# Optimization experiments

Measured on AMD Instinct MI355X. Metric: run time of the kernel, lower is better.

Reference implementation:

```python
import jax, jax.numpy as jnp
import numpy as np

S = 4  # upsample scale


def setup_inputs() -> dict:
    key = jax.random.key(0)
    ks = jax.random.split(key, 8)
    B, C, H, W = 4, 128, 64, 64
    feat_lr = jax.random.normal(ks[0], (B, C, H, W), dtype=jnp.float32)
    # gate: Conv2d(C, C//4, 1, bias=False) -> LeakyReLU(0.2) -> Conv2d(C//4, 1, 1, bias=True) -> Sigmoid
    gate_w1 = jax.random.normal(ks[1], (C, C // 4), dtype=jnp.float32) * 0.05
    gate_w2 = jax.random.normal(ks[2], (C // 4, 1), dtype=jnp.float32) * 0.1
    gate_b2 = jnp.full((1,), -3.0, dtype=jnp.float32)  # init bias per module
    # mlp: Conv2d(C+2, C, 1) -> ReLU -> Conv2d(C, C, 1)
    mlp_w1 = jax.random.normal(ks[3], (C + 2, C), dtype=jnp.float32) * 0.05
    mlp_b1 = jax.random.normal(ks[4], (C,), dtype=jnp.float32) * 0.01
    mlp_w2 = jax.random.normal(ks[5], (C, C), dtype=jnp.float32) * 0.05
    mlp_b2 = jax.random.normal(ks[6], (C,), dtype=jnp.float32) * 0.01
    return {"feat_lr": feat_lr, "gate_w1": gate_w1, "gate_w2": gate_w2,
            "gate_b2": gate_b2, "mlp_w1": mlp_w1, "mlp_b1": mlp_b1,
            "mlp_w2": mlp_w2, "mlp_b2": mlp_b2}


def reference(feat_lr, gate_w1, gate_w2, gate_b2, mlp_w1, mlp_b1, mlp_w2, mlp_b2):
    B, C, H, W = feat_lr.shape
    f = jnp.transpose(feat_lr, (0, 2, 3, 1))  # (B,H,W,C)

    # ---- gate on LR grid (1x1 convs == per-pixel matmuls) ----
    g = f @ gate_w1                              # (B,H,W,C//4)
    g = jnp.where(g >= 0, g, 0.2 * g)            # LeakyReLU(0.2)
    gate = jax.nn.sigmoid(g @ gate_w2 + gate_b2) # (B,H,W,1)

    # ---- subpixel grid: channels [x, y], values in (-1,1) ----
    coords = jnp.linspace(-1.0 + 1.0 / S, 1.0 - 1.0 / S, S, dtype=feat_lr.dtype)
    yy, xx = jnp.meshgrid(coords, coords, indexing="ij")
    grid = jnp.stack([xx, yy], axis=-1)          # (S,S,2)

    # ---- mlp: split first conv weight into feat part and grid part.
    # Since convs are 1x1 and feat_hr is nearest-upsampled (constant over each
    # SxS block) while grid tiles per block, hidden = relu(f@W1f + grid@W1g + b1)
    # broadcast over (block, subpixel) — avoids materializing concat/HR inputs.
    w1_f, w1_g = mlp_w1[:C], mlp_w1[C:]          # (C,C), (2,C)
    h_f = f @ w1_f                               # (B,H,W,C)
    h_g = grid @ w1_g                            # (S,S,C)
    hidden = jax.nn.relu(h_f[:, :, None, :, None, :]
                         + h_g[None, None, :, None, :, :]
                         + mlp_b1)               # (B,H,S,W,S,C)
    res = hidden @ mlp_w2 + mlp_b2               # (B,H,S,W,S,C)

    out = res * gate[:, :, None, :, None, :]     # broadcast gate over block
    out = out.reshape(B, H * S, W * S, C)
    return jnp.transpose(out, (0, 3, 1, 2))      # (B,C,H*S,W*S)
```

## Files before the change

kernel.cpp:

```cpp
#include <hip/hip_runtime.h>
#include <hip/hip_bf16.h>
#include <math.h>


typedef __attribute__((ext_vector_type(8))) short bf16x8;
typedef __attribute__((ext_vector_type(4))) float f32x4;

__device__ inline short f2bf(float v) {
    __hip_bfloat16 b = __float2bfloat16(v);
    return *reinterpret_cast<short*>(&b);
}

__global__ __launch_bounds__(256) void w2t_kernel(const float* __restrict__ w2,
                                                  __hip_bfloat16* __restrict__ w2t) {
    __shared__ float tile[16][17];
    const int kt = (blockIdx.x & 7) * 16, jt = (blockIdx.x >> 3) * 16;
    const int tx = threadIdx.x & 15, ty = threadIdx.x >> 4;
    tile[ty][tx] = w2[(kt + ty) * 128 + jt + tx];
    __syncthreads();
    w2t[(jt + ty) * 128 + kt + tx] = __float2bfloat16(tile[tx][ty]);
}

__global__ __launch_bounds__(256, 3) void ipi_kernel(
    const float* __restrict__ feat,
    const float* __restrict__ gate_w1,
    const float* __restrict__ gate_w2,
    const float* __restrict__ gate_b2,
    const float* __restrict__ mlp_w1,
    const float* __restrict__ mlp_b1,
    const float* __restrict__ mlp_b2,
    const __hip_bfloat16* __restrict__ w2t,
    float* __restrict__ out)
{
    __shared__ float hf[16 * 132];
    __shared__ float hgb[16 * 132];
    __shared__ float gate_s[16];
    __shared__ char  hid[32768];
    float* f_tile = (float*)hid;
    float* glds   = (float*)(hid + 8192);

    const int t    = threadIdx.x;
    const int lane = t & 63;
    const int wv   = t >> 6;
    const int bx   = blockIdx.x;
    const int w0   = (bx & 3) * 16;
    const int h    = (bx >> 2) & 63;
    const int b    = bx >> 8;

    bf16x8 afrag[2][4];
    f32x4  b2v[2];
    {
        const __hip_bfloat16* base = w2t + (wv * 32 + (lane & 15)) * 128 + (lane >> 4) * 8;
        #pragma unroll
        for (int jt = 0; jt < 2; ++jt) {
            #pragma unroll
            for (int ks = 0; ks < 4; ++ks)
                afrag[jt][ks] = *(const bf16x8*)(base + jt * 16 * 128 + ks * 32);
            b2v[jt] = *(const f32x4*)&mlp_b2[wv * 32 + jt * 16 + (lane >> 4) * 4];
        }
    }

    {
        const float* fbase = feat + ((size_t)(b * 128) * 64 + h) * 64 + w0;
        #pragma unroll
        for (int i = 0; i < 8; ++i) {
            int idx = t + i * 256;
            int c = idx >> 4, w = idx & 15;
            f_tile[c * 16 + w] = fbase[(size_t)c * 4096 + w];
        }
        #pragma unroll
        for (int i = 0; i < 8; ++i) {
            int idx = t + i * 256;
            int s = idx >> 7, k = idx & 127;
            float cx = -0.75f + 0.5f * (float)(s & 3);
            float cy = -0.75f + 0.5f * (float)(s >> 2);
            hgb[s * 132 + k] = cx * mlp_w1[128 * 128 + k]
                             + cy * mlp_w1[129 * 128 + k]
                             + mlp_b1[k];
        }
    }
    __syncthreads();

    {
        int jg = t & 31, wq = t >> 5;
        float a0 = 0.f, a1 = 0.f;
        for (int c = 0; c < 128; ++c) {
            float gw = gate_w1[c * 32 + jg];
            a0 = fmaf(f_tile[c * 16 + wq], gw, a0);
            a1 = fmaf(f_tile[c * 16 + wq + 8], gw, a1);
        }
        glds[wq * 32 + jg]       = (a0 >= 0.f) ? a0 : 0.2f * a0;
        glds[(wq + 8) * 32 + jg] = (a1 >= 0.f) ? a1 : 0.2f * a1;
    }

    {
        int j = t & 127, wb = t >> 7;
        float acc[8];
        #pragma unroll
        for (int i = 0; i < 8; ++i) acc[i] = 0.f;
        for (int c = 0; c < 128; ++c) {
            float wvv = mlp_w1[c * 128 + j];
            const float4* fp = (const float4*)&f_tile[c * 16 + wb * 8];
            float4 fa = fp[0], fb = fp[1];
            acc[0] = fmaf(fa.x, wvv, acc[0]);
            acc[1] = fmaf(fa.y, wvv, acc[1]);
            acc[2] = fmaf(fa.z, wvv, acc[2]);
            acc[3] = fmaf(fa.w, wvv, acc[3]);
            acc[4] = fmaf(fb.x, wvv, acc[4]);
            acc[5] = fmaf(fb.y, wvv, acc[5]);
            acc[6] = fmaf(fb.z, wvv, acc[6]);
            acc[7] = fmaf(fb.w, wvv, acc[7]);
        }
        #pragma unroll
        for (int i = 0; i < 8; ++i) hf[(wb * 8 + i) * 132 + j] = acc[i];
    }
    __syncthreads();

    if (t < 16) {
        float s = gate_b2[0];
        for (int jg = 0; jg < 32; ++jg) s += glds[t * 32 + jg] * gate_w2[jg];
        gate_s[t] = 1.f / (1.f + expf(-s));
    }

    for (int half = 0; half < 2; ++half) {
        __syncthreads();

        {
            const int mh = t >> 1;
            const int w  = (mh >> 2) & 15;
            const int s  = ((((half << 7) + mh) >> 6) << 2) | (mh & 3);
            const float* hfr = hf  + w * 132 + (t & 1) * 64;
            const float* hgr = hgb + s * 132 + (t & 1) * 64;
            char* rowp = hid + mh * 256;
            const int kb0 = (t & 1) * 128;
            const int sw  = (mh & 7) << 4;
            #pragma unroll
            for (int kc = 0; kc < 8; ++kc) {
                float4 a0 = *(const float4*)(hfr + kc * 8);
                float4 a1 = *(const float4*)(hfr + kc * 8 + 4);
                float4 g0 = *(const float4*)(hgr + kc * 8);
                float4 g1 = *(const float4*)(hgr + kc * 8 + 4);
                bf16x8 hv;
                hv[0] = f2bf(fmaxf(a0.x + g0.x, 0.f));
                hv[1] = f2bf(fmaxf(a0.y + g0.y, 0.f));
                hv[2] = f2bf(fmaxf(a0.z + g0.z, 0.f));
                hv[3] = f2bf(fmaxf(a0.w + g0.w, 0.f));
                hv[4] = f2bf(fmaxf(a1.x + g1.x, 0.f));
                hv[5] = f2bf(fmaxf(a1.y + g1.y, 0.f));
                hv[6] = f2bf(fmaxf(a1.z + g1.z, 0.f));
                hv[7] = f2bf(fmaxf(a1.w + g1.w, 0.f));
                *(bf16x8*)(rowp + ((kb0 + kc * 16) ^ sw)) = hv;
            }
        }
        __syncthreads();

        for (int mt = 0; mt < 8; ++mt) {
            const int mrow = mt * 16 + (lane & 15);
            const int swb  = (mrow & 7) << 4;
            const char* rowp = hid + mrow * 256;
            bf16x8 bfrag[4];
            #pragma unroll
            for (int ks = 0; ks < 4; ++ks)
                bfrag[ks] = *(const bf16x8*)(rowp + ((ks * 64 + (lane >> 4) * 16) ^ swb));

            f32x4 acc0 = {0.f, 0.f, 0.f, 0.f};
            f32x4 acc1 = {0.f, 0.f, 0.f, 0.f};
            #pragma unroll
            for (int ks = 0; ks < 4; ++ks) {
                acc0 = __builtin_amdgcn_mfma_f32_16x16x32_bf16(afrag[0][ks], bfrag[ks], acc0, 0, 0, 0);
                acc1 = __builtin_amdgcn_mfma_f32_16x16x32_bf16(afrag[1][ks], bfrag[ks], acc1, 0, 0, 0);
            }

            const int m  = (half << 7) + mrow;
            const int sy = m >> 6;
            const float g = gate_s[(m >> 2) & 15];
            float* outp = out + ((size_t)(b * 128 + wv * 32 + (lane >> 4) * 4) << 16)
                              + (size_t)(h * 4 + sy) * 256 + w0 * 4 + (m & 63);
            #pragma unroll
            for (int r = 0; r < 4; ++r) {
                outp[(size_t)r << 16]        = (acc0[r] + b2v[0][r]) * g;
                outp[(size_t)(r + 16) << 16] = (acc1[r] + b2v[1][r]) * g;
            }
        }
    }
}

extern "C" void kernel_launch(void* const* d_in, const int* in_sizes, int n_in,
                              void* d_out, int out_size, void* d_ws, size_t ws_size,
                              hipStream_t stream) {
    const float* feat = (const float*)d_in[0];
    const float* gw1  = (const float*)d_in[1];
    const float* gw2  = (const float*)d_in[2];
    const float* gb2  = (const float*)d_in[3];
    const float* w1   = (const float*)d_in[4];
    const float* b1   = (const float*)d_in[5];
    const float* w2   = (const float*)d_in[6];
    const float* b2   = (const float*)d_in[7];
    float* o = (float*)d_out;
    __hip_bfloat16* w2t = (__hip_bfloat16*)d_ws;

    w2t_kernel<<<dim3(64), dim3(256), 0, stream>>>(w2, w2t);
    ipi_kernel<<<dim3(1024), dim3(256), 0, stream>>>(feat, gw1, gw2, gb2, w1, b1, b2, w2t, o);
}
```

Baseline: 55.35 us.

## Split fused kernel into staging and MFMA main kernels via workspace

Splits the fused kernel into two launches. A stage kernel computes the per-pixel first-layer MLP output, the gate, the grid bias term and the transposed bf16 W2, and writes them to workspace. A main kernel reads those values from global memory, builds the hidden tile in LDS and runs the MFMA GEMM. The aim is lower LDS and register use per kernel so occupancy can rise to 4 blocks per CU, and fewer launches by folding the W2 transpose into the stage kernel. The cost is an extra round trip of roughly 8 MB through global memory for hf, and it falls back to the old monolithic path if the workspace is too small.

```diff
diff --git a/kernel.cpp b/kernel.cpp
--- a/kernel.cpp
+++ b/kernel.cpp
@@ -11,72 +11,58 @@
     return *reinterpret_cast<short*>(&b);
 }
 
-__global__ __launch_bounds__(256) void w2t_kernel(const float* __restrict__ w2,
-                                                  __hip_bfloat16* __restrict__ w2t) {
-    __shared__ float tile[16][17];
-    const int kt = (blockIdx.x & 7) * 16, jt = (blockIdx.x >> 3) * 16;
-    const int tx = threadIdx.x & 15, ty = threadIdx.x >> 4;
-    tile[ty][tx] = w2[(kt + ty) * 128 + jt + tx];
-    __syncthreads();
-    w2t[(jt + ty) * 128 + kt + tx] = __float2bfloat16(tile[tx][ty]);
-}
-
-__global__ __launch_bounds__(256, 3) void ipi_kernel(
+__device__ inline void barrier_lgkm() {
+    asm volatile("s_waitcnt lgkmcnt(0)" ::: "memory");
+    __builtin_amdgcn_s_barrier();
+    asm volatile("" ::: "memory");
+}
+
+__global__ __launch_bounds__(256, 4) void ipi_stage_kernel(
     const float* __restrict__ feat,
     const float* __restrict__ gate_w1,
     const float* __restrict__ gate_w2,
     const float* __restrict__ gate_b2,
     const float* __restrict__ mlp_w1,
     const float* __restrict__ mlp_b1,
-    const float* __restrict__ mlp_b2,
-    const __hip_bfloat16* __restrict__ w2t,
-    float* __restrict__ out)
+    const float* __restrict__ w2,
+    float* __restrict__ hf_ws,
+    float* __restrict__ gate_ws,
+    float* __restrict__ hgb_ws,
+    __hip_bfloat16* __restrict__ w2t)
 {
-    __shared__ float hf[16 * 132];
-    __shared__ float hgb[16 * 132];
-    __shared__ float gate_s[16];
-    __shared__ char  hid[32768];
-    float* f_tile = (float*)hid;
-    float* glds   = (float*)(hid + 8192);
-
-    const int t    = threadIdx.x;
-    const int lane = t & 63;
-    const int wv   = t >> 6;
-    const int bx   = blockIdx.x;
-    const int w0   = (bx & 3) * 16;
-    const int h    = (bx >> 2) & 63;
-    const int b    = bx >> 8;
-
-    bf16x8 afrag[2][4];
-    f32x4  b2v[2];
-    {
-        const __hip_bfloat16* base = w2t + (wv * 32 + (lane & 15)) * 128 + (lane >> 4) * 8;
-        #pragma unroll
-        for (int jt = 0; jt < 2; ++jt) {
-            #pragma unroll
-            for (int ks = 0; ks < 4; ++ks)
-                afrag[jt][ks] = *(const bf16x8*)(base + jt * 16 * 128 + ks * 32);
-            b2v[jt] = *(const f32x4*)&mlp_b2[wv * 32 + jt * 16 + (lane >> 4) * 4];
-        }
-    }
-
-    {
-        const float* fbase = feat + ((size_t)(b * 128) * 64 + h) * 64 + w0;
-        #pragma unroll
-        for (int i = 0; i < 8; ++i) {
-            int idx = t + i * 256;
-            int c = idx >> 4, w = idx & 15;
-            f_tile[c * 16 + w] = fbase[(size_t)c * 4096 + w];
-        }
+    __shared__ float f_tile[128 * 16];
+    __shared__ float glds[16 * 32];
+
+    const int t  = threadIdx.x;
+    const int bx = blockIdx.x;
+    const int w0 = (bx & 3) * 16;
+    const int h  = (bx >> 2) & 63;
+    const int b  = bx >> 8;
+
+    if (bx == 0) {
         #pragma unroll
         for (int i = 0; i < 8; ++i) {
             int idx = t + i * 256;
             int s = idx >> 7, k = idx & 127;
             float cx = -0.75f + 0.5f * (float)(s & 3);
             float cy = -0.75f + 0.5f * (float)(s >> 2);
-            hgb[s * 132 + k] = cx * mlp_w1[128 * 128 + k]
-                             + cy * mlp_w1[129 * 128 + k]
-                             + mlp_b1[k];
+            hgb_ws[idx] = cx * mlp_w1[128 * 128 + k]
+                        + cy * mlp_w1[129 * 128 + k]
+                        + mlp_b1[k];
+        }
+    } else if (bx <= 64) {
+        int gid = (bx - 1) * 256 + t;
+        int j = gid >> 7, k = gid & 127;
+        w2t[gid] = __float2bfloat16(w2[k * 128 + j]);
+    }
+
+    {
+        const float* fbase = feat + ((size_t)(b * 128) * 64 + h) * 64 + w0;
+        #pragma unroll
+        for (int i = 0; i < 8; ++i) {
+            int idx = t + i * 256;
+            int c = idx >> 4, w = idx & 15;
+            f_tile[c * 16 + w] = fbase[(size_t)c * 4096 + w];
         }
     }
     __syncthreads();
@@ -111,26 +97,62 @@
             acc[6] = fmaf(fb.z, wvv, acc[6]);
             acc[7] = fmaf(fb.w, wvv, acc[7]);
         }
-        #pragma unroll
-        for (int i = 0; i < 8; ++i) hf[(wb * 8 + i) * 132 + j] = acc[i];
+        float* hfb = hf_ws + ((size_t)((b * 64 + h) * 64) + w0 + wb * 8) * 128 + j;
+        #pragma unroll
+        for (int i = 0; i < 8; ++i) hfb[i * 128] = acc[i];
     }
     __syncthreads();
 
     if (t < 16) {
         float s = gate_b2[0];
         for (int jg = 0; jg < 32; ++jg) s += glds[t * 32 + jg] * gate_w2[jg];
-        gate_s[t] = 1.f / (1.f + expf(-s));
-    }
+        gate_ws[(b * 64 + h) * 64 + w0 + t] = 1.f / (1.f + expf(-s));
+    }
+}
+
+__global__ __launch_bounds__(256, 4) void ipi_main_kernel(
+    const __hip_bfloat16* __restrict__ w2t,
+    const float* __restrict__ mlp_b2,
+    const float* __restrict__ hf_ws,
+    const float* __restrict__ gate_ws,
+    const float* __restrict__ hgb_ws,
+    float* __restrict__ out)
+{
+    __shared__ char hid[32768];
+
+    const int t    = threadIdx.x;
+    const int lane = t & 63;
+    const int wv   = t >> 6;
+    const int bx   = blockIdx.x;
+    const int w0   = (bx & 3) * 16;
+    const int h    = (bx >> 2) & 63;
+    const int b    = bx >> 8;
+
+    bf16x8 afrag[2][4];
+    f32x4  b2v[2];
+    {
+        const __hip_bfloat16* base = w2t + (wv * 32 + (lane & 15)) * 128 + (lane >> 4) * 8;
+        #pragma unroll
+        for (int jt = 0; jt < 2; ++jt) {
+            #pragma unroll
+            for (int ks = 0; ks < 4; ++ks)
+                afrag[jt][ks] = *(const bf16x8*)(base + jt * 16 * 128 + ks * 32);
+            b2v[jt] = *(const f32x4*)&mlp_b2[wv * 32 + jt * 16 + (lane >> 4) * 4];
+        }
+    }
+
+    const float* hfbase = hf_ws + ((size_t)((b * 64 + h) * 64) + w0) * 128;
+    const float* gbase  = gate_ws + (b * 64 + h) * 64 + w0;
 
     for (int half = 0; half < 2; ++half) {
-        __syncthreads();
+        barrier_lgkm();
 
         {
             const int mh = t >> 1;
             const int w  = (mh >> 2) & 15;
-            const int s  = ((((half << 7) + mh) >> 6) << 2) | (mh & 3);
-            const float* hfr = hf  + w * 132 + (t & 1) * 64;
-            const float* hgr = hgb + s * 132 + (t & 1) * 64;
+            const int s  = (((half << 1) + (mh >> 6)) << 2) | (mh & 3);
+            const float* hfr = hfbase + w * 128 + (t & 1) * 64;
+            const float* hgr = hgb_ws + s * 128 + (t & 1) * 64;
             char* rowp = hid + mh * 256;
             const int kb0 = (t & 1) * 128;
             const int sw  = (mh & 7) << 4;
@@ -152,7 +174,7 @@
                 *(bf16x8*)(rowp + ((kb0 + kc * 16) ^ sw)) = hv;
             }
         }
-        __syncthreads();
+        barrier_lgkm();
 
         for (int mt = 0; mt < 8; ++mt) {
             const int mrow = mt * 16 + (lane & 15);
@@ -171,6 +193,166 @@
                 acc1 = __builtin_amdgcn_mfma_f32_16x16x32_bf16(afrag[1][ks], bfrag[ks], acc1, 0, 0, 0);
             }
 
+            const int m  = (half << 7) + mrow;
+            const int sy = m >> 6;
+            const float g = gbase[(m >> 2) & 15];
+            float* outp = out + ((size_t)(b * 128 + wv * 32 + (lane >> 4) * 4) << 16)
+                              + (size_t)(h * 4 + sy) * 256 + w0 * 4 + (m & 63);
+            #pragma unroll
+            for (int r = 0; r < 4; ++r) {
+                outp[(size_t)r << 16]        = (acc0[r] + b2v[0][r]) * g;
+                outp[(size_t)(r + 16) << 16] = (acc1[r] + b2v[1][r]) * g;
+            }
+        }
+    }
+}
+
+__global__ __launch_bounds__(256) void w2t_kernel(const float* __restrict__ w2,
+                                                  __hip_bfloat16* __restrict__ w2t) {
+    __shared__ float tile[16][17];
+    const int kt = (blockIdx.x & 7) * 16, jt = (blockIdx.x >> 3) * 16;
+    const int tx = threadIdx.x & 15, ty = threadIdx.x >> 4;
+    tile[ty][tx] = w2[(kt + ty) * 128 + jt + tx];
+    __syncthreads();
+    w2t[(jt + ty) * 128 + kt + tx] = __float2bfloat16(tile[tx][ty]);
+}
+
+__global__ __launch_bounds__(256, 3) void ipi_mono_kernel(
+    const float* __restrict__ feat, const float* __restrict__ gate_w1,
+    const float* __restrict__ gate_w2, const float* __restrict__ gate_b2,
+    const float* __restrict__ mlp_w1, const float* __restrict__ mlp_b1,
+    const float* __restrict__ mlp_b2, const __hip_bfloat16* __restrict__ w2t,
+    float* __restrict__ out)
+{
+    __shared__ float hf[16 * 132];
+    __shared__ float hgb[16 * 132];
+    __shared__ float gate_s[16];
+    __shared__ char  hid[32768];
+    float* f_tile = (float*)hid;
+    float* glds   = (float*)(hid + 8192);
+
+    const int t    = threadIdx.x;
+    const int lane = t & 63;
+    const int wv   = t >> 6;
+    const int bx   = blockIdx.x;
+    const int w0   = (bx & 3) * 16;
+    const int h    = (bx >> 2) & 63;
+    const int b    = bx >> 8;
+
+    bf16x8 afrag[2][4];
+    f32x4  b2v[2];
+    {
+        const __hip_bfloat16* base = w2t + (wv * 32 + (lane & 15)) * 128 + (lane >> 4) * 8;
+        #pragma unroll
+        for (int jt = 0; jt < 2; ++jt) {
+            #pragma unroll
+            for (int ks = 0; ks < 4; ++ks)
+                afrag[jt][ks] = *(const bf16x8*)(base + jt * 16 * 128 + ks * 32);
+            b2v[jt] = *(const f32x4*)&mlp_b2[wv * 32 + jt * 16 + (lane >> 4) * 4];
+        }
+    }
+    {
+        const float* fbase = feat + ((size_t)(b * 128) * 64 + h) * 64 + w0;
+        #pragma unroll
+        for (int i = 0; i < 8; ++i) {
+            int idx = t + i * 256;
+            int c = idx >> 4, w = idx & 15;
+            f_tile[c * 16 + w] = fbase[(size_t)c * 4096 + w];
+        }
+        #pragma unroll
+        for (int i = 0; i < 8; ++i) {
+            int idx = t + i * 256;
+            int s = idx >> 7, k = idx & 127;
+            float cx = -0.75f + 0.5f * (float)(s & 3);
+            float cy = -0.75f + 0.5f * (float)(s >> 2);
+            hgb[s * 132 + k] = cx * mlp_w1[128 * 128 + k]
+                             + cy * mlp_w1[129 * 128 + k] + mlp_b1[k];
+        }
+    }
+    __syncthreads();
+    {
+        int jg = t & 31, wq = t >> 5;
+        float a0 = 0.f, a1 = 0.f;
+        for (int c = 0; c < 128; ++c) {
+            float gw = gate_w1[c * 32 + jg];
+            a0 = fmaf(f_tile[c * 16 + wq], gw, a0);
+            a1 = fmaf(f_tile[c * 16 + wq + 8], gw, a1);
+        }
+        glds[wq * 32 + jg]       = (a0 >= 0.f) ? a0 : 0.2f * a0;
+        glds[(wq + 8) * 32 + jg] = (a1 >= 0.f) ? a1 : 0.2f * a1;
+    }
+    {
+        int j = t & 127, wb = t >> 7;
+        float acc[8];
+        #pragma unroll
+        for (int i = 0; i < 8; ++i) acc[i] = 0.f;
+        for (int c = 0; c < 128; ++c) {
+            float wvv = mlp_w1[c * 128 + j];
+            const float4* fp = (const float4*)&f_tile[c * 16 + wb * 8];
+            float4 fa = fp[0], fb = fp[1];
+            acc[0] = fmaf(fa.x, wvv, acc[0]);
+            acc[1] = fmaf(fa.y, wvv, acc[1]);
+            acc[2] = fmaf(fa.z, wvv, acc[2]);
+            acc[3] = fmaf(fa.w, wvv, acc[3]);
+            acc[4] = fmaf(fb.x, wvv, acc[4]);
+            acc[5] = fmaf(fb.y, wvv, acc[5]);
+            acc[6] = fmaf(fb.z, wvv, acc[6]);
+            acc[7] = fmaf(fb.w, wvv, acc[7]);
+        }
+        #pragma unroll
+        for (int i = 0; i < 8; ++i) hf[(wb * 8 + i) * 132 + j] = acc[i];
+    }
+    __syncthreads();
+    if (t < 16) {
+        float s = gate_b2[0];
+        for (int jg = 0; jg < 32; ++jg) s += glds[t * 32 + jg] * gate_w2[jg];
+        gate_s[t] = 1.f / (1.f + expf(-s));
+    }
+    for (int half = 0; half < 2; ++half) {
+        __syncthreads();
+        {
+            const int mh = t >> 1;
+            const int w  = (mh >> 2) & 15;
+            const int s  = ((((half << 7) + mh) >> 6) << 2) | (mh & 3);
+            const float* hfr = hf  + w * 132 + (t & 1) * 64;
+            const float* hgr = hgb + s * 132 + (t & 1) * 64;
+            char* rowp = hid + mh * 256;
+            const int kb0 = (t & 1) * 128;
+            const int sw  = (mh & 7) << 4;
+            #pragma unroll
+            for (int kc = 0; kc < 8; ++kc) {
+                float4 a0 = *(const float4*)(hfr + kc * 8);
+                float4 a1 = *(const float4*)(hfr + kc * 8 + 4);
+                float4 g0 = *(const float4*)(hgr + kc * 8);
+                float4 g1 = *(const float4*)(hgr + kc * 8 + 4);
+                bf16x8 hv;
+                hv[0] = f2bf(fmaxf(a0.x + g0.x, 0.f));
+                hv[1] = f2bf(fmaxf(a0.y + g0.y, 0.f));
+                hv[2] = f2bf(fmaxf(a0.z + g0.z, 0.f));
+                hv[3] = f2bf(fmaxf(a0.w + g0.w, 0.f));
+                hv[4] = f2bf(fmaxf(a1.x + g1.x, 0.f));
+                hv[5] = f2bf(fmaxf(a1.y + g1.y, 0.f));
+                hv[6] = f2bf(fmaxf(a1.z + g1.z, 0.f));
+                hv[7] = f2bf(fmaxf(a1.w + g1.w, 0.f));
+                *(bf16x8*)(rowp + ((kb0 + kc * 16) ^ sw)) = hv;
+            }
+        }
+        __syncthreads();
+        for (int mt = 0; mt < 8; ++mt) {
+            const int mrow = mt * 16 + (lane & 15);
+            const int swb  = (mrow & 7) << 4;
+            const char* rowp = hid + mrow * 256;
+            bf16x8 bfrag[4];
+            #pragma unroll
+            for (int ks = 0; ks < 4; ++ks)
+                bfrag[ks] = *(const bf16x8*)(rowp + ((ks * 64 + (lane >> 4) * 16) ^ swb));
+            f32x4 acc0 = {0.f, 0.f, 0.f, 0.f};
+            f32x4 acc1 = {0.f, 0.f, 0.f, 0.f};
+            #pragma unroll
+            for (int ks = 0; ks < 4; ++ks) {
+                acc0 = __builtin_amdgcn_mfma_f32_16x16x32_bf16(afrag[0][ks], bfrag[ks], acc0, 0, 0, 0);
+                acc1 = __builtin_amdgcn_mfma_f32_16x16x32_bf16(afrag[1][ks], bfrag[ks], acc1, 0, 0, 0);
+            }
             const int m  = (half << 7) + mrow;
             const int sy = m >> 6;
             const float g = gate_s[(m >> 2) & 15];
@@ -197,8 +379,26 @@
     const float* w2   = (const float*)d_in[6];
     const float* b2   = (const float*)d_in[7];
     float* o = (float*)d_out;
-    __hip_bfloat16* w2t = (__hip_bfloat16*)d_ws;
-
-    w2t_kernel<<<dim3(64), dim3(256), 0, stream>>>(w2, w2t);
-    ipi_kernel<<<dim3(1024), dim3(256), 0, stream>>>(feat, gw1, gw2, gb2, w1, b1, b2, w2t, o);
-}
+
+    const size_t OFF_HF   = 32768;
+    const size_t OFF_GATE = OFF_HF + (size_t)4 * 64 * 64 * 128 * 4;
+    const size_t OFF_HGB  = OFF_GATE + (size_t)4 * 64 * 64 * 4;
+    const size_t NEED     = OFF_HGB + 16 * 128 * 4;
+
+    char* ws = (char*)d_ws;
+    __hip_bfloat16* w2t = (__hip_bfloat16*)ws;
+
+    if (ws_size >= NEED) {
+        float* hf_ws   = (float*)(ws + OFF_HF);
+        float* gate_ws = (float*)(ws + OFF_GATE);
+        float* hgb_ws  = (float*)(ws + OFF_HGB);
+        ipi_stage_kernel<<<dim3(1024), dim3(256), 0, stream>>>(
+            feat, gw1, gw2, gb2, w1, b1, w2, hf_ws, gate_ws, hgb_ws, w2t);
+        ipi_main_kernel<<<dim3(1024), dim3(256), 0, stream>>>(
+            w2t, b2, hf_ws, gate_ws, hgb_ws, o);
+    } else {
+        w2t_kernel<<<dim3(64), dim3(256), 0, stream>>>(w2, w2t);
+        ipi_mono_kernel<<<dim3(1024), dim3(256), 0, stream>>>(
+            feat, gw1, gw2, gb2, w1, b1, b2, w2t, o);
+    }
+}
```

After: 65.98 us. 19.2% more time.

## Move LR-grid projections to split-bf16 MFMA and shrink hidden tile to quarters

Applied to the files above, without the earlier changes.

Replaces the scalar FP32 loops computing f@W1f and the gate's first conv with MFMA bf16 matmuls. Precision is kept by a hi/lo bf16 split (three MFMAs per step), and the weight split and transpose are precomputed in a merged prep kernel. The hidden tile is built and consumed in four quarters of 64 rows instead of two halves of 128, halving LDS to allow launch_bounds occupancy 4. Barriers are swapped for an lgkmcnt wait plus s_barrier. This trades extra barriers and global reads of the split weights for removing the scalar FMA bottleneck.

```diff
diff --git a/kernel.cpp b/kernel.cpp
--- a/kernel.cpp
+++ b/kernel.cpp
@@ -11,36 +11,67 @@
     return *reinterpret_cast<short*>(&b);
 }
 
-__global__ __launch_bounds__(256) void w2t_kernel(const float* __restrict__ w2,
-                                                  __hip_bfloat16* __restrict__ w2t) {
-    __shared__ float tile[16][17];
-    const int kt = (blockIdx.x & 7) * 16, jt = (blockIdx.x >> 3) * 16;
-    const int tx = threadIdx.x & 15, ty = threadIdx.x >> 4;
-    tile[ty][tx] = w2[(kt + ty) * 128 + jt + tx];
-    __syncthreads();
-    w2t[(jt + ty) * 128 + kt + tx] = __float2bfloat16(tile[tx][ty]);
-}
-
-__global__ __launch_bounds__(256, 3) void ipi_kernel(
+__device__ inline void barrier_lgkm() {
+    asm volatile("s_waitcnt lgkmcnt(0)" ::: "memory");
+    __builtin_amdgcn_s_barrier();
+    asm volatile("" ::: "memory");
+}
+
+__global__ __launch_bounds__(256) void ipi_pre_kernel(
+    const float* __restrict__ w2,
+    const float* __restrict__ w1,
+    const float* __restrict__ gw1,
+    __hip_bfloat16* __restrict__ w2t,
+    __hip_bfloat16* __restrict__ w1t_hi,
+    __hip_bfloat16* __restrict__ w1t_lo,
+    __hip_bfloat16* __restrict__ g1t_hi,
+    __hip_bfloat16* __restrict__ g1t_lo)
+{
+    int gid = blockIdx.x * 256 + threadIdx.x;
+    if (gid < 16384) {
+        int j = gid >> 7, k = gid & 127;
+        w2t[gid] = __float2bfloat16(w2[k * 128 + j]);
+    } else if (gid < 32768) {
+        int i = gid - 16384, j = i >> 7, c = i & 127;
+        float v = w1[c * 128 + j];
+        __hip_bfloat16 hi = __float2bfloat16(v);
+        w1t_hi[i] = hi;
+        w1t_lo[i] = __float2bfloat16(v - __bfloat162float(hi));
+    } else if (gid < 36864) {
+        int i = gid - 32768, jg = i >> 7, c = i & 127;
+        float v = gw1[c * 32 + jg];
+        __hip_bfloat16 hi = __float2bfloat16(v);
+        g1t_hi[i] = hi;
+        g1t_lo[i] = __float2bfloat16(v - __bfloat162float(hi));
+    }
+}
+
+__global__ __launch_bounds__(256, 4) void ipi_main(
     const float* __restrict__ feat,
-    const float* __restrict__ gate_w1,
+    const float* __restrict__ mlp_w1,
+    const float* __restrict__ mlp_b1,
     const float* __restrict__ gate_w2,
     const float* __restrict__ gate_b2,
-    const float* __restrict__ mlp_w1,
-    const float* __restrict__ mlp_b1,
     const float* __restrict__ mlp_b2,
     const __hip_bfloat16* __restrict__ w2t,
+    const __hip_bfloat16* __restrict__ w1t_hi,
+    const __hip_bfloat16* __restrict__ w1t_lo,
+    const __hip_bfloat16* __restrict__ g1t_hi,
+    const __hip_bfloat16* __restrict__ g1t_lo,
     float* __restrict__ out)
 {
-    __shared__ float hf[16 * 132];
-    __shared__ float hgb[16 * 132];
+    __shared__ float hf_s[16 * 132];
+    __shared__ float hgb_s[16 * 132];
     __shared__ float gate_s[16];
-    __shared__ char  hid[32768];
-    float* f_tile = (float*)hid;
-    float* glds   = (float*)(hid + 8192);
+    __shared__ char  hid[16384];
+    short* f_hi = (short*)hid;
+    short* f_lo = (short*)(hid + 4352);
+    float* glds = (float*)(hid + 8704);
 
     const int t    = threadIdx.x;
     const int lane = t & 63;
+    const int lg   = lane >> 4;
+    const int ml   = lane & 15;
     const int wv   = t >> 6;
     const int bx   = blockIdx.x;
     const int w0   = (bx & 3) * 16;
@@ -50,13 +81,13 @@
     bf16x8 afrag[2][4];
     f32x4  b2v[2];
     {
-        const __hip_bfloat16* base = w2t + (wv * 32 + (lane & 15)) * 128 + (lane >> 4) * 8;
+        const __hip_bfloat16* base = w2t + (wv * 32 + ml) * 128 + lg * 8;
         #pragma unroll
         for (int jt = 0; jt < 2; ++jt) {
             #pragma unroll
             for (int ks = 0; ks < 4; ++ks)
-                afrag[jt][ks] = *(const bf16x8*)(base + jt * 16 * 128 + ks * 32);
-            b2v[jt] = *(const f32x4*)&mlp_b2[wv * 32 + jt * 16 + (lane >> 4) * 4];
+                afrag[jt][ks] = *(const bf16x8*)(base + jt * 2048 + ks * 32);
+            b2v[jt] = *(const f32x4*)&mlp_b2[wv * 32 + jt * 16 + lg * 4];
         }
     }
 
@@ -66,7 +97,11 @@
         for (int i = 0; i < 8; ++i) {
             int idx = t + i * 256;
             int c = idx >> 4, w = idx & 15;
-            f_tile[c * 16 + w] = fbase[(size_t)c * 4096 + w];
+            float v = fbase[(size_t)c * 4096 + w];
+            short hi = f2bf(v);
+            float hf32 = __bfloat162float(*(__hip_bfloat16*)&hi);
+            f_hi[w * 136 + c] = hi;
+            f_lo[w * 136 + c] = f2bf(v - hf32);
         }
         #pragma unroll
         for (int i = 0; i < 8; ++i) {
@@ -74,68 +109,85 @@
             int s = idx >> 7, k = idx & 127;
             float cx = -0.75f + 0.5f * (float)(s & 3);
             float cy = -0.75f + 0.5f * (float)(s >> 2);
-            hgb[s * 132 + k] = cx * mlp_w1[128 * 128 + k]
-                             + cy * mlp_w1[129 * 128 + k]
-                             + mlp_b1[k];
-        }
-    }
-    __syncthreads();
+            hgb_s[s * 132 + k] = cx * mlp_w1[16384 + k]
+                               + cy * mlp_w1[16512 + k] + mlp_b1[k];
+        }
+    }
+    barrier_lgkm();
 
     {
-        int jg = t & 31, wq = t >> 5;
-        float a0 = 0.f, a1 = 0.f;
-        for (int c = 0; c < 128; ++c) {
-            float gw = gate_w1[c * 32 + jg];
-            a0 = fmaf(f_tile[c * 16 + wq], gw, a0);
-            a1 = fmaf(f_tile[c * 16 + wq + 8], gw, a1);
-        }
-        glds[wq * 32 + jg]       = (a0 >= 0.f) ? a0 : 0.2f * a0;
-        glds[(wq + 8) * 32 + jg] = (a1 >= 0.f) ? a1 : 0.2f * a1;
-    }
-
-    {
-        int j = t & 127, wb = t >> 7;
-        float acc[8];
-        #pragma unroll
-        for (int i = 0; i < 8; ++i) acc[i] = 0.f;
-        for (int c = 0; c < 128; ++c) {
-            float wvv = mlp_w1[c * 128 + j];
-            const float4* fp = (const float4*)&f_tile[c * 16 + wb * 8];
-            float4 fa = fp[0], fb = fp[1];
-            acc[0] = fmaf(fa.x, wvv, acc[0]);
-            acc[1] = fmaf(fa.y, wvv, acc[1]);
-            acc[2] = fmaf(fa.z, wvv, acc[2]);
-            acc[3] = fmaf(fa.w, wvv, acc[3]);
-            acc[4] = fmaf(fb.x, wvv, acc[4]);
-            acc[5] = fmaf(fb.y, wvv, acc[5]);
-            acc[6] = fmaf(fb.z, wvv, acc[6]);
-            acc[7] = fmaf(fb.w, wvv, acc[7]);
-        }
-        #pragma unroll
-        for (int i = 0; i < 8; ++i) hf[(wb * 8 + i) * 132 + j] = acc[i];
-    }
-    __syncthreads();
+        bf16x8 fhi[4], flo[4];
+        {
+            const short* fb  = f_hi + ml * 136 + lg * 8;
+            const short* flb = f_lo + ml * 136 + lg * 8;
+            #pragma unroll
+            for (int ks = 0; ks < 4; ++ks) {
+                fhi[ks] = *(const bf16x8*)(fb + ks * 32);
+                flo[ks] = *(const bf16x8*)(flb + ks * 32);
+            }
+        }
+        #pragma unroll
+        for (int jj = 0; jj < 2; ++jj) {
+            const int jt16 = (wv * 2 + jj) * 16;
+            const __hip_bfloat16* bh = w1t_hi + (jt16 + ml) * 128 + lg * 8;
+            const __hip_bfloat16* bl = w1t_lo + (jt16 + ml) * 128 + lg * 8;
+            f32x4 acc = {0.f, 0.f, 0.f, 0.f};
+            #pragma unroll
+            for (int ks = 0; ks < 4; ++ks) {
+                bf16x8 Bh = *(const bf16x8*)(bh + ks * 32);
+                bf16x8 Bl = *(const bf16x8*)(bl + ks * 32);
+                acc = __builtin_amdgcn_mfma_f32_16x16x32_bf16(fhi[ks], Bh, acc, 0, 0, 0);
+                acc = __builtin_amdgcn_mfma_f32_16x16x32_bf16(fhi[ks], Bl, acc, 0, 0, 0);
+                acc = __builtin_amdgcn_mfma_f32_16x16x32_bf16(flo[ks], Bh, acc, 0, 0, 0);
+            }
+            #pragma unroll
+            for (int r = 0; r < 4; ++r)
+                hf_s[(lg * 4 + r) * 132 + jt16 + ml] = acc[r];
+        }
+        if (wv == 0) {
+            #pragma unroll
+            for (int jt = 0; jt < 2; ++jt) {
+                const __hip_bfloat16* bh = g1t_hi + (jt * 16 + ml) * 128 + lg * 8;
+                const __hip_bfloat16* bl = g1t_lo + (jt * 16 + ml) * 128 + lg * 8;
+                f32x4 acc = {0.f, 0.f, 0.f, 0.f};
+                #pragma unroll
+                for (int ks = 0; ks < 4; ++ks) {
+                    bf16x8 Bh = *(const bf16x8*)(bh + ks * 32);
+                    bf16x8 Bl = *(const bf16x8*)(bl + ks * 32);
+                    acc = __builtin_amdgcn_mfma_f32_16x16x32_bf16(fhi[ks], Bh, acc, 0, 0, 0);
+                    acc = __builtin_amdgcn_mfma_f32_16x16x32_bf16(fhi[ks], Bl, acc, 0, 0, 0);
+                    acc = __builtin_amdgcn_mfma_f32_16x16x32_bf16(flo[ks], Bh, acc, 0, 0, 0);
+                }
+                #pragma unroll
+                for (int r = 0; r < 4; ++r) {
+                    float v = acc[r];
+                    glds[(lg * 4 + r) * 33 + jt * 16 + ml] = (v >= 0.f) ? v : 0.2f * v;
+                }
+            }
+        }
+    }
+    barrier_lgkm();
 
     if (t < 16) {
         float s = gate_b2[0];
-        for (int jg = 0; jg < 32; ++jg) s += glds[t * 32 + jg] * gate_w2[jg];
+        #pragma unroll 8
+        for (int jg = 0; jg < 32; ++jg) s = fmaf(glds[t * 33 + jg], gate_w2[jg], s);
         gate_s[t] = 1.f / (1.f + expf(-s));
     }
-
-    for (int half = 0; half < 2; ++half) {
-        __syncthreads();
-
+    barrier_lgkm();
+
+    const int mq  = t >> 2;
+    const int wA  = mq >> 2;
+    const int sxA = mq & 3;
+    const int kq  = t & 3;
+    for (int q = 0; q < 4; ++q) {
         {
-            const int mh = t >> 1;
-            const int w  = (mh >> 2) & 15;
-            const int s  = ((((half << 7) + mh) >> 6) << 2) | (mh & 3);
-            const float* hfr = hf  + w * 132 + (t & 1) * 64;
-            const float* hgr = hgb + s * 132 + (t & 1) * 64;
-            char* rowp = hid + mh * 256;
-            const int kb0 = (t & 1) * 128;
-            const int sw  = (mh & 7) << 4;
-            #pragma unroll
-            for (int kc = 0; kc < 8; ++kc) {
+            const float* hfr = hf_s  + wA * 132 + kq * 32;
+            const float* hgr = hgb_s + (q * 4 + sxA) * 132 + kq * 32;
+            char* rowp = hid + mq * 256;
+            const int sw = (mq & 7) << 4;
+            #pragma unroll
+            for (int kc = 0; kc < 4; ++kc) {
                 float4 a0 = *(const float4*)(hfr + kc * 8);
                 float4 a1 = *(const float4*)(hfr + kc * 8 + 4);
                 float4 g0 = *(const float4*)(hgr + kc * 8);
@@ -149,19 +201,20 @@
                 hv[5] = f2bf(fmaxf(a1.y + g1.y, 0.f));
                 hv[6] = f2bf(fmaxf(a1.z + g1.z, 0.f));
                 hv[7] = f2bf(fmaxf(a1.w + g1.w, 0.f));
-                *(bf16x8*)(rowp + ((kb0 + kc * 16) ^ sw)) = hv;
-            }
-        }
-        __syncthreads();
-
-        for (int mt = 0; mt < 8; ++mt) {
-            const int mrow = mt * 16 + (lane & 15);
+                *(bf16x8*)(rowp + ((kq * 64 + kc * 16) ^ sw)) = hv;
+            }
+        }
+        barrier_lgkm();
+
+        #pragma unroll
+        for (int mt = 0; mt < 4; ++mt) {
+            const int mrow = mt * 16 + ml;
             const int swb  = (mrow & 7) << 4;
             const char* rowp = hid + mrow * 256;
             bf16x8 bfrag[4];
             #pragma unroll
             for (int ks = 0; ks < 4; ++ks)
-                bfrag[ks] = *(const bf16x8*)(rowp + ((ks * 64 + (lane >> 4) * 16) ^ swb));
+                bfrag[ks] = *(const bf16x8*)(rowp + ((ks * 64 + lg * 16) ^ swb));
 
             f32x4 acc0 = {0.f, 0.f, 0.f, 0.f};
             f32x4 acc1 = {0.f, 0.f, 0.f, 0.f};
@@ -171,17 +224,16 @@
                 acc1 = __builtin_amdgcn_mfma_f32_16x16x32_bf16(afrag[1][ks], bfrag[ks], acc1, 0, 0, 0);
             }
 
-            const int m  = (half << 7) + mrow;
-            const int sy = m >> 6;
-            const float g = gate_s[(m >> 2) & 15];
-            float* outp = out + ((size_t)(b * 128 + wv * 32 + (lane >> 4) * 4) << 16)
-                              + (size_t)(h * 4 + sy) * 256 + w0 * 4 + (m & 63);
+            const float g = gate_s[mrow >> 2];
+            float* outp = out + ((size_t)(b * 128 + wv * 32 + lg * 4) << 16)
+                              + (size_t)(h * 4 + q) * 256 + w0 * 4 + mrow;
             #pragma unroll
             for (int r = 0; r < 4; ++r) {
                 outp[(size_t)r << 16]        = (acc0[r] + b2v[0][r]) * g;
                 outp[(size_t)(r + 16) << 16] = (acc1[r] + b2v[1][r]) * g;
             }
         }
+        barrier_lgkm();
     }
 }
 
@@ -197,8 +249,16 @@
     const float* w2   = (const float*)d_in[6];
     const float* b2   = (const float*)d_in[7];
     float* o = (float*)d_out;
-    __hip_bfloat16* w2t = (__hip_bfloat16*)d_ws;
-
-    w2t_kernel<<<dim3(64), dim3(256), 0, stream>>>(w2, w2t);
-    ipi_kernel<<<dim3(1024), dim3(256), 0, stream>>>(feat, gw1, gw2, gb2, w1, b1, b2, w2t, o);
-}
+
+    char* ws = (char*)d_ws;
+    __hip_bfloat16* w2t    = (__hip_bfloat16*)(ws);
+    __hip_bfloat16* w1t_hi = (__hip_bfloat16*)(ws + 32768);
+    __hip_bfloat16* w1t_lo = (__hip_bfloat16*)(ws + 65536);
+    __hip_bfloat16* g1t_hi = (__hip_bfloat16*)(ws + 98304);
+    __hip_bfloat16* g1t_lo = (__hip_bfloat16*)(ws + 106496);
+
+    ipi_pre_kernel<<<dim3(144), dim3(256), 0, stream>>>(
+        w2, w1, gw1, w2t, w1t_hi, w1t_lo, g1t_hi, g1t_lo);
+    ipi_main<<<dim3(1024), dim3(256), 0, stream>>>(
+        feat, w1, b1, gw2, gb2, b2, w2t, w1t_hi, w1t_lo, g1t_hi, g1t_lo, o);
+}
```

Result: faster. 44.36 us (-19.8%).
